# Performance work log

Measured on AMD Instinct MI355X. Metric: run time of the kernel, lower is better.

Reference implementation:

```python
import jax, jax.numpy as jnp
import numpy as np

TOPK = 9
NUM_CLASSES = 80
EPS = 1e-9


def setup_inputs() -> dict:
    key = jax.random.key(0)
    k1, k2, k3, k4 = jax.random.split(key, 4)
    B, G, C = 32, 32, NUM_CLASSES
    IMG = 640.0
    # anchor priors over strides 8/16/32 for a 640x640 image -> 6400+1600+400
    levels = []
    for stride, fs in ((8, 80), (16, 40), (32, 20)):
        ys, xs = jnp.meshgrid(jnp.arange(fs, dtype=jnp.float32),
                              jnp.arange(fs, dtype=jnp.float32), indexing='ij')
        cx = (xs.reshape(-1) + 0.5) * stride
        cy = (ys.reshape(-1) + 0.5) * stride
        half = stride * 2.5
        levels.append(jnp.stack([cx - half, cy - half, cx + half, cy + half], axis=1))
    priors = jnp.concatenate(levels, axis=0).astype(jnp.float32)  # (8400,4)

    def rand_boxes(k, shape):
        kc, ks = jax.random.split(k)
        c = jax.random.uniform(kc, shape + (2,), minval=40.0, maxval=IMG - 40.0)
        s = jax.random.uniform(ks, shape + (2,), minval=20.0, maxval=160.0)
        return jnp.concatenate([c - s / 2, c + s / 2], axis=-1).astype(jnp.float32)

    gt_bboxes = rand_boxes(k1, (B, G))
    pred_bboxes = rand_boxes(k2, (B, 8400))
    gt_labels = jax.random.randint(k3, (B, G, 1), 0, C)
    pad_bbox_flag = (jax.random.uniform(k4, (B, G, 1)) < 0.8).astype(jnp.float32)
    return {
        'priors': priors,
        'num_level_priors': [6400, 1600, 400],
        'gt_labels': gt_labels,
        'gt_bboxes': gt_bboxes,
        'pad_bbox_flag': pad_bbox_flag,
        'pred_bboxes': pred_bboxes,
    }


def _atss(priors, num_level_priors, gt_labels, gt_bboxes, pad_bbox_flag, pred_bboxes):
    B, G = gt_bboxes.shape[:2]
    P = priors.shape[0]

    # --- pairwise IoU gt vs priors (mmdet BboxOverlaps2D), shape (B,G,P) ---
    gt_flat = gt_bboxes.reshape(-1, 4)
    lt = jnp.maximum(gt_flat[:, None, :2], priors[None, :, :2])
    rb = jnp.minimum(gt_flat[:, None, 2:], priors[None, :, 2:])
    wh = jnp.clip(rb - lt, 0)
    inter = wh[..., 0] * wh[..., 1]
    area_g = (gt_flat[:, 2] - gt_flat[:, 0]) * (gt_flat[:, 3] - gt_flat[:, 1])
    area_p = (priors[:, 2] - priors[:, 0]) * (priors[:, 3] - priors[:, 1])
    union = jnp.maximum(area_g[:, None] + area_p[None, :] - inter, 1e-6)
    overlaps = (inter / union).reshape(B, G, P)

    # --- center distances (B,G,P) ---
    gt_c = (gt_flat[:, :2] + gt_flat[:, 2:]) / 2.0
    pr_c = (priors[:, :2] + priors[:, 2:]) / 2.0
    distances = jnp.sqrt(((gt_c[:, None, :] - pr_c[None, :, :]) ** 2).sum(-1)).reshape(B, G, P)

    # --- per-level topk candidate selection (smallest center distance) ---
    pad_bool = pad_bbox_flag > 0  # (B,G,1)
    is_in_candidate, candidate_idxs = [], []
    start = 0
    for n in num_level_priors:
        n = int(n)
        d = distances[..., start:start + n]
        k = min(TOPK, n)
        _, idx = jax.lax.top_k(-d, k)                      # (B,G,k)
        candidate_idxs.append(idx + start)
        idx = jnp.where(pad_bool, idx, 0)
        counts = jax.nn.one_hot(idx, n, dtype=distances.dtype).sum(-2)  # (B,G,n)
        is_in_candidate.append(jnp.where(counts > 1, 0.0, counts))
        start += n
    is_in_candidate = jnp.concatenate(is_in_candidate, axis=-1)  # (B,G,P)
    candidate_idxs = jnp.concatenate(candidate_idxs, axis=-1)    # (B,G,K)

    # --- adaptive threshold: mean + std (ddof=1) of candidate IoUs per gt ---
    cand_overlaps_full = jnp.where(is_in_candidate > 0, overlaps, 0.0)
    cand = jnp.take_along_axis(cand_overlaps_full, candidate_idxs, axis=-1)  # (B,G,K)
    thr = cand.mean(-1, keepdims=True) + jnp.std(cand, axis=-1, keepdims=True, ddof=1)
    is_pos = jnp.where(cand_overlaps_full > thr, is_in_candidate, 0.0)

    # --- prior centers strictly inside gt boxes (B,G,P) ---
    deltas = jnp.concatenate([
        pr_c[None, None] - gt_bboxes[:, :, None, :2],
        gt_bboxes[:, :, None, 2:] - pr_c[None, None]], axis=-1)
    is_in_gts = (deltas.min(-1) > EPS).astype(gt_bboxes.dtype)

    pos_mask = is_pos * is_in_gts * pad_bbox_flag  # (B,G,P)

    # --- resolve priors assigned to multiple gts by highest IoU ---
    fg = pos_mask.sum(1)                                   # (B,P)
    multi = fg[:, None, :] > 1
    best_gt = jnp.argmax(overlaps, axis=1)                 # (B,P)
    is_max = jnp.transpose(jax.nn.one_hot(best_gt, G, dtype=overlaps.dtype), (0, 2, 1))
    pos_mask = jnp.where(multi, is_max, pos_mask)
    fg_mask = pos_mask.sum(1)                              # (B,P)
    gt_idx = jnp.argmax(pos_mask, axis=1)                  # (B,P)

    # --- gather targets ---
    labels = jnp.take_along_axis(gt_labels[..., 0], gt_idx, axis=1)  # (B,P)
    labels = jnp.where(fg_mask > 0, labels, NUM_CLASSES)
    boxes = jnp.take_along_axis(gt_bboxes, jnp.broadcast_to(gt_idx[:, :, None], (B, P, 4)), axis=1)
    scores = jax.nn.one_hot(labels, NUM_CLASSES + 1, dtype=gt_bboxes.dtype)[..., :NUM_CLASSES]

    # --- scale scores by IoU(gt, pred) restricted to positive assignments ---
    lt2 = jnp.maximum(gt_bboxes[:, :, None, :2], pred_bboxes[:, None, :, :2])
    rb2 = jnp.minimum(gt_bboxes[:, :, None, 2:], pred_bboxes[:, None, :, 2:])
    inter2 = jnp.clip(rb2 - lt2, 0).prod(-1)
    a_g = jnp.clip(gt_bboxes[..., 2:] - gt_bboxes[..., :2], 0).prod(-1)
    a_p = jnp.clip(pred_bboxes[..., 2:] - pred_bboxes[..., :2], 0).prod(-1)
    ious = inter2 / (a_g[:, :, None] + a_p[:, None, :] - inter2 + EPS)
    ious = (ious * pos_mask).max(1)[..., None]             # (B,P,1)
    scores = scores * ious

    return labels.astype(jnp.int32), boxes, scores, fg_mask > 0


def reference(priors, num_level_priors, gt_labels, gt_bboxes, pad_bbox_flag, pred_bboxes):
    return _atss(priors, num_level_priors, gt_labels, gt_bboxes, pad_bbox_flag, pred_bboxes)
```

## Files before the change

### kernel.cpp

```cpp
#include <hip/hip_runtime.h>
#include <math.h>

#define B 32
#define G 32
#define P 8400
#define NC 80
#define NCAND 27
#define INFF 3.4e38f

__device__ __forceinline__ float iou_prior(float gx1, float gy1, float gx2, float gy2, float4 pr) {
    float ltx = fmaxf(gx1, pr.x), lty = fmaxf(gy1, pr.y);
    float rbx = fminf(gx2, pr.z), rby = fminf(gy2, pr.w);
    float w = fmaxf(rbx - ltx, 0.f), h = fmaxf(rby - lty, 0.f);
    float inter = w * h;
    float ag = (gx2 - gx1) * (gy2 - gy1);
    float ap = (pr.z - pr.x) * (pr.w - pr.y);
    float uni = fmaxf(ag + ap - inter, 1e-6f);
    return inter / uni;
}

__global__ __launch_bounds__(64) void k_cand(const float4* __restrict__ priors,
                                             const float4* __restrict__ gtb,
                                             const float* __restrict__ flagv,
                                             int* __restrict__ cand_idx,
                                             float* __restrict__ cand_pos,
                                             float4* __restrict__ rec) {
    __shared__ int cslot[NCAND];
    const int bg = blockIdx.x;
    const int lane = threadIdx.x;

    for (int i = bg * 64 + lane; i < B * P; i += B * G * 64)
        rec[i] = make_float4(0.f, 0.f, 0.f, 0.f);

    if (flagv[bg] <= 0.f) {
        if (lane < NCAND) { cand_idx[bg * NCAND + lane] = 0; cand_pos[bg * NCAND + lane] = 0.f; }
        return;
    }

    float4 gt = gtb[bg];
    float gcx = (gt.x + gt.z) * 0.5f, gcy = (gt.y + gt.w) * 0.5f;

    const int   starts[3] = {0, 6400, 8000};
    const int   fsz[3]    = {80, 40, 20};
    const float inv[3]    = {0.125f, 0.0625f, 0.03125f};

    const int c7 = lane % 7, r7 = lane / 7;

    for (int l = 0; l < 3; ++l) {
        int fs = fsz[l];
        int x0 = (int)(gcx * inv[l]);
        int y0 = (int)(gcy * inv[l]);
        int xs = min(max(x0 - 3, 0), fs - 7);
        int ys = min(max(y0 - 3, 0), fs - 7);

        float v = INFF; int pi = 0x7fffffff;
        if (lane < 49) {
            int col = xs + c7, row = ys + r7;
            pi = starts[l] + row * fs + col;
            float4 pr = priors[pi];
            float dx = gcx - (pr.x + pr.z) * 0.5f;
            float dy = gcy - (pr.y + pr.w) * 0.5f;
            v = sqrtf(dx * dx + dy * dy);
        }
        int rank = 0;
        for (int j = 0; j < 49; ++j) {
            float ov = __shfl(v, j, 64);
            int   oi = __shfl(pi, j, 64);
            rank += (ov < v || (ov == v && oi < pi)) ? 1 : 0;
        }
        if (lane < 49 && rank < 9) cslot[l * 9 + rank] = pi;
    }
    __syncthreads();

    float covv = 0.f; int cingv = 0; int myIdx = 0;
    if (lane < NCAND) {
        myIdx = cslot[lane];
        float4 pr = priors[myIdx];
        covv = iou_prior(gt.x, gt.y, gt.z, gt.w, pr);
        float pcx = (pr.x + pr.z) * 0.5f, pcy = (pr.y + pr.w) * 0.5f;
        float m = fminf(fminf(pcx - gt.x, pcy - gt.y), fminf(gt.z - pcx, gt.w - pcy));
        cingv = (m > 1e-9f) ? 1 : 0;
    }
    float s = 0.f;
    for (int j = 0; j < NCAND; ++j) s += __shfl(covv, j, 64);
    float mean = s / (float)NCAND;
    float d = covv - mean;
    float d2 = (lane < NCAND) ? d * d : 0.f;
    float vs = 0.f;
    for (int j = 0; j < NCAND; ++j) vs += __shfl(d2, j, 64);
    float thr = mean + sqrtf(vs / (float)(NCAND - 1));

    if (lane < NCAND) {
        cand_idx[bg * NCAND + lane] = myIdx;
        cand_pos[bg * NCAND + lane] = (covv > thr && cingv) ? 1.f : 0.f;
    }
}

__global__ __launch_bounds__(896) void k_resolve(const float4* __restrict__ priors,
                                                 const float4* __restrict__ gtb,
                                                 const float4* __restrict__ predb,
                                                 const int* __restrict__ gtl,
                                                 const int* __restrict__ cand_idx,
                                                 const float* __restrict__ cand_pos,
                                                 float4* __restrict__ rec) {
    __shared__ int cnt[P];
    const int b = blockIdx.x;
    const int t = threadIdx.x;

    for (int i = t; i < P; i += 896) cnt[i] = 0;
    __syncthreads();

    const int base = b * G * NCAND;
    const int e = t;
    bool active = (e < G * NCAND) && (cand_pos[base + e] > 0.f);
    int p = 0;
    if (active) {
        p = cand_idx[base + e];
        atomicAdd(&cnt[p], 1);
    }
    __syncthreads();

    if (active) {
        int gi = e / NCAND;
        if (cnt[p] > 1) {
            float4 pr = priors[p];
            float best = -1.f; gi = 0;
            for (int g2 = 0; g2 < G; ++g2) {
                float4 gt2 = gtb[b * G + g2];
                float ov = iou_prior(gt2.x, gt2.y, gt2.z, gt2.w, pr);
                if (ov > best) { best = ov; gi = g2; }
            }
        }
        float4 gt = gtb[b * G + gi];
        float4 pd = predb[b * P + p];
        float ltx = fmaxf(gt.x, pd.x), lty = fmaxf(gt.y, pd.y);
        float rbx = fminf(gt.z, pd.z), rby = fminf(gt.w, pd.w);
        float iw = fmaxf(rbx - ltx, 0.f), ih = fmaxf(rby - lty, 0.f);
        float inter = iw * ih;
        float ag = fmaxf(gt.z - gt.x, 0.f) * fmaxf(gt.w - gt.y, 0.f);
        float ap = fmaxf(pd.z - pd.x, 0.f) * fmaxf(pd.w - pd.y, 0.f);
        float iou = inter / (ag + ap - inter + 1e-9f);
        int lab = gtl[b * G + gi];
        rec[b * P + p] = make_float4(1.f, (float)gi, iou, (float)lab);
    }
}

__global__ __launch_bounds__(256) void k_scores(const float4* __restrict__ rec,
                                                float4* __restrict__ scores) {
    int tid = blockIdx.x * 256 + threadIdx.x;
    int bp = tid / 20;
    int q = tid % 20;
    float4 r = rec[bp];
    float4 o = make_float4(0.f, 0.f, 0.f, 0.f);
    if (r.x > 0.f) {
        int lab = (int)r.w;
        int c0 = q * 4;
        if (lab >= c0 && lab < c0 + 4) {
            (&o.x)[lab - c0] = r.z;
        }
    }
    scores[tid] = o;
}

__global__ __launch_bounds__(256) void k_misc(const float4* __restrict__ rec,
                                              const float4* __restrict__ gtb,
                                              float* __restrict__ labels,
                                              float4* __restrict__ boxes,
                                              float* __restrict__ fgm) {
    int bp = blockIdx.x * 256 + threadIdx.x;
    int b = bp / P;
    float4 r = rec[bp];
    bool fg = r.x > 0.f;
    int gi = fg ? (int)r.y : 0;
    labels[bp] = fg ? r.w : (float)NC;
    boxes[bp] = gtb[b * G + gi];
    fgm[bp] = fg ? 1.f : 0.f;
}

extern "C" void kernel_launch(void* const* d_in, const int* in_sizes, int n_in,
                              void* d_out, int out_size, void* d_ws, size_t ws_size,
                              hipStream_t stream) {
    const float4* priors = (const float4*)d_in[0];
    const int*    gtl    = (const int*)d_in[2];
    const float4* gtb    = (const float4*)d_in[3];
    const float*  flagv  = (const float*)d_in[4];
    const float4* predb  = (const float4*)d_in[5];

    char* wsb = (char*)d_ws;
    float4* rec      = (float4*)wsb;
    int*    cand_idx = (int*)(wsb + (size_t)B * P * 16);
    float*  cand_pos = (float*)(wsb + (size_t)B * P * 16 + (size_t)B * G * NCAND * 4);

    float*  out    = (float*)d_out;
    float*  labels = out;
    float4* boxes  = (float4*)(out + B * P);
    float4* scores = (float4*)(out + B * P + B * P * 4);
    float*  fgm    = out + B * P + B * P * 4 + B * P * NC;

    hipLaunchKernelGGL(k_cand,    dim3(B * G),            dim3(64),  0, stream, priors, gtb, flagv, cand_idx, cand_pos, rec);
    hipLaunchKernelGGL(k_resolve, dim3(B),                dim3(896), 0, stream, priors, gtb, predb, gtl, cand_idx, cand_pos, rec);
    hipLaunchKernelGGL(k_scores,  dim3(B * P * 20 / 256), dim3(256), 0, stream, rec, scores);
    hipLaunchKernelGGL(k_misc,    dim3(B * P / 256),      dim3(256), 0, stream, rec, gtb, labels, boxes, fgm);
}
```

Before: 71.57 us.

## Fuse candidate selection with resolve and merge output kernels using a fg bitmask

Merges candidate selection and overlap resolution into one per-batch kernel, with one wave per GT and the candidates held in shared memory. This removes a launch and the global round-trip for the candidates. The full zeroing of the rec buffer is replaced by a per-batch foreground bitmask, so rec is only read where the mask bit is set. The score and misc output kernels are merged into one. The trade-off is that the assign stage now runs on only 32 blocks, with each wave handling two GTs serially.

```diff
diff --git a/kernel.cpp b/kernel.cpp
--- a/kernel.cpp
+++ b/kernel.cpp
@@ -7,6 +7,7 @@
 #define NC 80
 #define NCAND 27
 #define INFF 3.4e38f
+#define MWPI 264
 
 __device__ __forceinline__ float iou_prior(float gx1, float gy1, float gx2, float gy2, float4 pr) {
     float ltx = fmaxf(gx1, pr.x), lty = fmaxf(gy1, pr.y);
@@ -19,109 +20,91 @@
     return inter / uni;
 }
 
-__global__ __launch_bounds__(64) void k_cand(const float4* __restrict__ priors,
-                                             const float4* __restrict__ gtb,
-                                             const float* __restrict__ flagv,
-                                             int* __restrict__ cand_idx,
-                                             float* __restrict__ cand_pos,
-                                             float4* __restrict__ rec) {
-    __shared__ int cslot[NCAND];
-    const int bg = blockIdx.x;
-    const int lane = threadIdx.x;
+__global__ __launch_bounds__(1024) void k_assign(const float4* __restrict__ priors,
+                                                 const float4* __restrict__ gtb,
+                                                 const float4* __restrict__ predb,
+                                                 const int* __restrict__ gtl,
+                                                 const float* __restrict__ flagv,
+                                                 float4* __restrict__ rec,
+                                                 unsigned int* __restrict__ mask) {
+    __shared__ int   cnt[P];
+    __shared__ int   s_ci[G * NCAND];
+    __shared__ float s_cp[G * NCAND];
+    const int b = blockIdx.x;
+    const int t = threadIdx.x;
+    const int wave = t >> 6, lane = t & 63;
 
-    for (int i = bg * 64 + lane; i < B * P; i += B * G * 64)
-        rec[i] = make_float4(0.f, 0.f, 0.f, 0.f);
-
-    if (flagv[bg] <= 0.f) {
-        if (lane < NCAND) { cand_idx[bg * NCAND + lane] = 0; cand_pos[bg * NCAND + lane] = 0.f; }
-        return;
-    }
-
-    float4 gt = gtb[bg];
-    float gcx = (gt.x + gt.z) * 0.5f, gcy = (gt.y + gt.w) * 0.5f;
+    for (int i = t; i < P; i += 1024) cnt[i] = 0;
+    if (t < MWPI) mask[b * MWPI + t] = 0u;
 
     const int   starts[3] = {0, 6400, 8000};
     const int   fsz[3]    = {80, 40, 20};
     const float inv[3]    = {0.125f, 0.0625f, 0.03125f};
-
     const int c7 = lane % 7, r7 = lane / 7;
 
-    for (int l = 0; l < 3; ++l) {
-        int fs = fsz[l];
-        int x0 = (int)(gcx * inv[l]);
-        int y0 = (int)(gcy * inv[l]);
-        int xs = min(max(x0 - 3, 0), fs - 7);
-        int ys = min(max(y0 - 3, 0), fs - 7);
+    for (int g = wave; g < G; g += 16) {
+        const int bg = b * G + g;
+        if (flagv[bg] <= 0.f) {
+            if (lane < NCAND) { s_ci[g * NCAND + lane] = 0; s_cp[g * NCAND + lane] = 0.f; }
+            continue;
+        }
+        float4 gt = gtb[bg];
+        float gcx = (gt.x + gt.z) * 0.5f, gcy = (gt.y + gt.w) * 0.5f;
 
-        float v = INFF; int pi = 0x7fffffff;
-        if (lane < 49) {
-            int col = xs + c7, row = ys + r7;
-            pi = starts[l] + row * fs + col;
-            float4 pr = priors[pi];
-            float dx = gcx - (pr.x + pr.z) * 0.5f;
-            float dy = gcy - (pr.y + pr.w) * 0.5f;
-            v = sqrtf(dx * dx + dy * dy);
+        for (int l = 0; l < 3; ++l) {
+            int fs = fsz[l];
+            int x0 = (int)(gcx * inv[l]);
+            int y0 = (int)(gcy * inv[l]);
+            int xs = min(max(x0 - 3, 0), fs - 7);
+            int ys = min(max(y0 - 3, 0), fs - 7);
+
+            float v = INFF; int pi = 0x7fffffff;
+            if (lane < 49) {
+                int col = xs + c7, row = ys + r7;
+                pi = starts[l] + row * fs + col;
+                float4 pr = priors[pi];
+                float dx = gcx - (pr.x + pr.z) * 0.5f;
+                float dy = gcy - (pr.y + pr.w) * 0.5f;
+                v = sqrtf(dx * dx + dy * dy);
+            }
+            int rank = 0;
+            for (int j = 0; j < 49; ++j) {
+                float ov = __shfl(v, j, 64);
+                int   oi = __shfl(pi, j, 64);
+                rank += (ov < v || (ov == v && oi < pi)) ? 1 : 0;
+            }
+            if (lane < 49 && rank < 9) s_ci[g * NCAND + l * 9 + rank] = pi;
         }
-        int rank = 0;
-        for (int j = 0; j < 49; ++j) {
-            float ov = __shfl(v, j, 64);
-            int   oi = __shfl(pi, j, 64);
-            rank += (ov < v || (ov == v && oi < pi)) ? 1 : 0;
+
+        float covv = 0.f; int cingv = 0;
+        if (lane < NCAND) {
+            int myIdx = s_ci[g * NCAND + lane];
+            float4 pr = priors[myIdx];
+            covv = iou_prior(gt.x, gt.y, gt.z, gt.w, pr);
+            float pcx = (pr.x + pr.z) * 0.5f, pcy = (pr.y + pr.w) * 0.5f;
+            float m = fminf(fminf(pcx - gt.x, pcy - gt.y), fminf(gt.z - pcx, gt.w - pcy));
+            cingv = (m > 1e-9f) ? 1 : 0;
         }
-        if (lane < 49 && rank < 9) cslot[l * 9 + rank] = pi;
+        float s = 0.f;
+        for (int j = 0; j < NCAND; ++j) s += __shfl(covv, j, 64);
+        float mean = s / (float)NCAND;
+        float d = covv - mean;
+        float d2 = (lane < NCAND) ? d * d : 0.f;
+        float vs = 0.f;
+        for (int j = 0; j < NCAND; ++j) vs += __shfl(d2, j, 64);
+        float thr = mean + sqrtf(vs / (float)(NCAND - 1));
+
+        if (lane < NCAND) s_cp[g * NCAND + lane] = (covv > thr && cingv) ? 1.f : 0.f;
     }
     __syncthreads();
 
-    float covv = 0.f; int cingv = 0; int myIdx = 0;
-    if (lane < NCAND) {
-        myIdx = cslot[lane];
-        float4 pr = priors[myIdx];
-        covv = iou_prior(gt.x, gt.y, gt.z, gt.w, pr);
-        float pcx = (pr.x + pr.z) * 0.5f, pcy = (pr.y + pr.w) * 0.5f;
-        float m = fminf(fminf(pcx - gt.x, pcy - gt.y), fminf(gt.z - pcx, gt.w - pcy));
-        cingv = (m > 1e-9f) ? 1 : 0;
-    }
-    float s = 0.f;
-    for (int j = 0; j < NCAND; ++j) s += __shfl(covv, j, 64);
-    float mean = s / (float)NCAND;
-    float d = covv - mean;
-    float d2 = (lane < NCAND) ? d * d : 0.f;
-    float vs = 0.f;
-    for (int j = 0; j < NCAND; ++j) vs += __shfl(d2, j, 64);
-    float thr = mean + sqrtf(vs / (float)(NCAND - 1));
-
-    if (lane < NCAND) {
-        cand_idx[bg * NCAND + lane] = myIdx;
-        cand_pos[bg * NCAND + lane] = (covv > thr && cingv) ? 1.f : 0.f;
-    }
-}
-
-__global__ __launch_bounds__(896) void k_resolve(const float4* __restrict__ priors,
-                                                 const float4* __restrict__ gtb,
-                                                 const float4* __restrict__ predb,
-                                                 const int* __restrict__ gtl,
-                                                 const int* __restrict__ cand_idx,
-                                                 const float* __restrict__ cand_pos,
-                                                 float4* __restrict__ rec) {
-    __shared__ int cnt[P];
-    const int b = blockIdx.x;
-    const int t = threadIdx.x;
-
-    for (int i = t; i < P; i += 896) cnt[i] = 0;
-    __syncthreads();
-
-    const int base = b * G * NCAND;
-    const int e = t;
-    bool active = (e < G * NCAND) && (cand_pos[base + e] > 0.f);
+    const bool active = (t < G * NCAND) && (s_cp[t] > 0.f);
     int p = 0;
-    if (active) {
-        p = cand_idx[base + e];
-        atomicAdd(&cnt[p], 1);
-    }
+    if (active) { p = s_ci[t]; atomicAdd(&cnt[p], 1); }
     __syncthreads();
 
     if (active) {
-        int gi = e / NCAND;
+        int gi = t / NCAND;
         if (cnt[p] > 1) {
             float4 pr = priors[p];
             float best = -1.f; gi = 0;
@@ -142,17 +125,27 @@
         float iou = inter / (ag + ap - inter + 1e-9f);
         int lab = gtl[b * G + gi];
         rec[b * P + p] = make_float4(1.f, (float)gi, iou, (float)lab);
+        atomicOr(&mask[b * MWPI + (p >> 5)], 1u << (p & 31));
     }
 }
 
-__global__ __launch_bounds__(256) void k_scores(const float4* __restrict__ rec,
-                                                float4* __restrict__ scores) {
+__global__ __launch_bounds__(256) void k_out(const float4* __restrict__ rec,
+                                             const unsigned int* __restrict__ mask,
+                                             const float4* __restrict__ gtb,
+                                             float* __restrict__ labels,
+                                             float4* __restrict__ boxes,
+                                             float4* __restrict__ scores,
+                                             float* __restrict__ fgm) {
     int tid = blockIdx.x * 256 + threadIdx.x;
     int bp = tid / 20;
-    int q = tid % 20;
-    float4 r = rec[bp];
+    int q = tid - bp * 20;
+    int b = bp / P;
+    int p = bp - b * P;
+    bool fg = (mask[b * MWPI + (p >> 5)] >> (p & 31)) & 1u;
+    float4 r = make_float4(0.f, 0.f, 0.f, 0.f);
     float4 o = make_float4(0.f, 0.f, 0.f, 0.f);
-    if (r.x > 0.f) {
+    if (fg) {
+        r = rec[bp];
         int lab = (int)r.w;
         int c0 = q * 4;
         if (lab >= c0 && lab < c0 + 4) {
@@ -160,21 +153,12 @@
         }
     }
     scores[tid] = o;
-}
-
-__global__ __launch_bounds__(256) void k_misc(const float4* __restrict__ rec,
-                                              const float4* __restrict__ gtb,
-                                              float* __restrict__ labels,
-                                              float4* __restrict__ boxes,
-                                              float* __restrict__ fgm) {
-    int bp = blockIdx.x * 256 + threadIdx.x;
-    int b = bp / P;
-    float4 r = rec[bp];
-    bool fg = r.x > 0.f;
-    int gi = fg ? (int)r.y : 0;
-    labels[bp] = fg ? r.w : (float)NC;
-    boxes[bp] = gtb[b * G + gi];
-    fgm[bp] = fg ? 1.f : 0.f;
+    if (q == 0) {
+        int gi = fg ? (int)r.y : 0;
+        labels[bp] = fg ? r.w : (float)NC;
+        boxes[bp] = gtb[b * G + gi];
+        fgm[bp] = fg ? 1.f : 0.f;
+    }
 }
 
 extern "C" void kernel_launch(void* const* d_in, const int* in_sizes, int n_in,
@@ -187,9 +171,8 @@
     const float4* predb  = (const float4*)d_in[5];
 
     char* wsb = (char*)d_ws;
-    float4* rec      = (float4*)wsb;
-    int*    cand_idx = (int*)(wsb + (size_t)B * P * 16);
-    float*  cand_pos = (float*)(wsb + (size_t)B * P * 16 + (size_t)B * G * NCAND * 4);
+    float4*       rec  = (float4*)wsb;
+    unsigned int* mask = (unsigned int*)(wsb + (size_t)B * P * 16);
 
     float*  out    = (float*)d_out;
     float*  labels = out;
@@ -197,8 +180,8 @@
     float4* scores = (float4*)(out + B * P + B * P * 4);
     float*  fgm    = out + B * P + B * P * 4 + B * P * NC;
 
-    hipLaunchKernelGGL(k_cand,    dim3(B * G),            dim3(64),  0, stream, priors, gtb, flagv, cand_idx, cand_pos, rec);
-    hipLaunchKernelGGL(k_resolve, dim3(B),                dim3(896), 0, stream, priors, gtb, predb, gtl, cand_idx, cand_pos, rec);
-    hipLaunchKernelGGL(k_scores,  dim3(B * P * 20 / 256), dim3(256), 0, stream, rec, scores);
-    hipLaunchKernelGGL(k_misc,    dim3(B * P / 256),      dim3(256), 0, stream, rec, gtb, labels, boxes, fgm);
+    hipLaunchKernelGGL(k_assign, dim3(B),                dim3(1024), 0, stream,
+                       priors, gtb, predb, gtl, flagv, rec, mask);
+    hipLaunchKernelGGL(k_out,    dim3(B * P * 20 / 256), dim3(256),  0, stream,
+                       rec, mask, gtb, labels, boxes, scores, fgm);
 }
```

After: 88.06 us. 23.1% more time.
